# Performance work log

Measured on AMD Instinct MI355X. Metric: run time of the kernel, lower is better.

Reference implementation:

```python
import jax, jax.numpy as jnp
import numpy as np


def setup_inputs() -> dict:
    key = jax.random.key(0)
    k1, k2, k3, k4 = jax.random.split(key, 4)
    B, IN, OUT, R = 4096, 4096, 4096, 256
    x = jax.random.normal(k1, (B, IN), dtype=jnp.float32)
    U = jax.random.normal(k2, (R, IN), dtype=jnp.float32) / np.sqrt(IN)
    V = jax.random.normal(k3, (OUT, R), dtype=jnp.float32) / np.sqrt(R)
    bias = jax.random.uniform(k4, (OUT,), dtype=jnp.float32,
                              minval=-IN ** -0.5, maxval=IN ** -0.5)
    return {"x": x, "U": U, "V": V, "bias": bias}


def reference(x, U, V, bias):
    # Low-rank linear: out[b,j] = sum_k V[j,k] * (sum_i U[k,i] * x[b,i]) + bias[j]
    # (the torch loops with sparsity=1.0 / keep_stride==1 compute exactly this)
    t = jnp.einsum('bi,ri->br', x, U)        # [B, R]
    out = jnp.einsum('br,or->bo', t, V) + bias  # [B, OUT]
    return out
```

## Files before the change

### kernel.cpp

```cpp
#include <hip/hip_runtime.h>

typedef __attribute__((ext_vector_type(8))) short bf16x8;
typedef __attribute__((ext_vector_type(4))) float f32x4;

__device__ __forceinline__ unsigned short f2bf(float f) {
  unsigned int u = __float_as_uint(f);
  return (unsigned short)((u + 0x7fffu + ((u >> 16) & 1u)) >> 16);
}

__device__ __forceinline__ void gload_lds16(const void* g, void* l) {
  __builtin_amdgcn_global_load_lds((const __attribute__((address_space(1))) void*)g,
                                   (__attribute__((address_space(3))) void*)l,
                                   16, 0, 0);
}

__global__ void cast3(const float4* __restrict__ x, const float4* __restrict__ U,
                      const float4* __restrict__ V, ushort4* __restrict__ xb,
                      ushort4* __restrict__ Ub, ushort4* __restrict__ Vb) {
  const int NX = 4096 * 4096 / 4;
  const int NU = 256 * 4096 / 4;
  int i = blockIdx.x * blockDim.x + threadIdx.x;
  int stride = gridDim.x * blockDim.x;
  for (; i < NX + 2 * NU; i += stride) {
    const float4* s; ushort4* d; int j;
    if (i < NX)           { s = x; d = xb; j = i; }
    else if (i < NX + NU) { s = U; d = Ub; j = i - NX; }
    else                  { s = V; d = Vb; j = i - NX - NU; }
    float4 v = s[j];
    ushort4 o;
    o.x = f2bf(v.x); o.y = f2bf(v.y); o.z = f2bf(v.z); o.w = f2bf(v.w);
    d[j] = o;
  }
}

template <int MREP, int NREP, bool BIAS>
__global__ __launch_bounds__(256)
void gemm_nt(const unsigned short* __restrict__ A,
             const unsigned short* __restrict__ B,
             const float* __restrict__ bias,
             float* __restrict__ C,
             int lda, int ldb, int ldc,
             int nkt, int kChunk, long long splitStride) {
  constexpr int BM = 32 * MREP;
  constexpr int BN = 32 * NREP;
  constexpr int ISS_A = BM / 64;
  constexpr int ISS_B = BN / 64;

  __shared__ unsigned short sA[2][BM * 32];
  __shared__ unsigned short sB[2][BN * 32];

  const int tid = threadIdx.x;
  const int l = tid & 63;
  const int w = tid >> 6;
  const int wm = (w >> 1) * (MREP * 16);
  const int wn = (w & 1) * (NREP * 16);
  const int rm = blockIdx.x * BM;
  const int rn = blockIdx.y * BN;
  const int k0base = blockIdx.z * kChunk;

  const int lr = l & 15;
  const int lc8 = (l >> 4) * 8;

  auto stage = [&](int kt, int buf) {
    const int k0 = k0base + kt * 32;
#pragma unroll
    for (int is = 0; is < ISS_A; ++is) {
      int eo = is * 2048 + tid * 8;
      int r = eo >> 5, c = eo & 31;
      gload_lds16(A + (long long)(rm + r) * lda + k0 + c, &sA[buf][eo]);
    }
#pragma unroll
    for (int is = 0; is < ISS_B; ++is) {
      int eo = is * 2048 + tid * 8;
      int r = eo >> 5, c = eo & 31;
      gload_lds16(B + (long long)(rn + r) * ldb + k0 + c, &sB[buf][eo]);
    }
  };

  f32x4 acc[MREP][NREP] = {};

  stage(0, 0);
  for (int kt = 0; kt < nkt; ++kt) {
    __syncthreads();
    if (kt + 1 < nkt) stage(kt + 1, (kt + 1) & 1);
    const unsigned short* a0 = sA[kt & 1];
    const unsigned short* b0 = sB[kt & 1];
    bf16x8 af[MREP], bfr[NREP];
#pragma unroll
    for (int m = 0; m < MREP; ++m)
      af[m] = *(const bf16x8*)&a0[(wm + m * 16 + lr) * 32 + lc8];
#pragma unroll
    for (int n = 0; n < NREP; ++n)
      bfr[n] = *(const bf16x8*)&b0[(wn + n * 16 + lr) * 32 + lc8];
#pragma unroll
    for (int m = 0; m < MREP; ++m)
#pragma unroll
      for (int n = 0; n < NREP; ++n)
        acc[m][n] = __builtin_amdgcn_mfma_f32_16x16x32_bf16(af[m], bfr[n], acc[m][n], 0, 0, 0);
  }

  float* Cb = C + (long long)blockIdx.z * splitStride;
  const int r0 = rm + wm + (l >> 4) * 4;
  const int c0 = rn + wn + lr;
#pragma unroll
  for (int n = 0; n < NREP; ++n) {
    const int cc = c0 + n * 16;
    const float badd = BIAS ? bias[cc] : 0.0f;
#pragma unroll
    for (int m = 0; m < MREP; ++m) {
#pragma unroll
      for (int i = 0; i < 4; ++i)
        Cb[(long long)(r0 + m * 16 + i) * ldc + cc] = acc[m][n][i] + badd;
    }
  }
}

__global__ void reduce4(const float4* __restrict__ P, ushort4* __restrict__ t) {
  const int S = 4096 * 256 / 4;
  int i = blockIdx.x * 256 + threadIdx.x;
  float4 a = P[i], b = P[i + S], c = P[i + 2 * S], d = P[i + 3 * S];
  ushort4 o;
  o.x = f2bf(a.x + b.x + c.x + d.x);
  o.y = f2bf(a.y + b.y + c.y + d.y);
  o.z = f2bf(a.z + b.z + c.z + d.z);
  o.w = f2bf(a.w + b.w + c.w + d.w);
  t[i] = o;
}

extern "C" void kernel_launch(void* const* d_in, const int* in_sizes, int n_in,
                              void* d_out, int out_size, void* d_ws, size_t ws_size,
                              hipStream_t stream) {
  const float* x    = (const float*)d_in[0];
  const float* U    = (const float*)d_in[1];
  const float* V    = (const float*)d_in[2];
  const float* bias = (const float*)d_in[3];
  float* out = (float*)d_out;

  char* ws = (char*)d_ws;
  float* P            = (float*)ws;
  unsigned short* tb  = (unsigned short*)(ws + (16u << 20));
  unsigned short* xb  = (unsigned short*)(ws + (18u << 20));
  unsigned short* Ub  = (unsigned short*)(ws + (50u << 20));
  unsigned short* Vb  = (unsigned short*)(ws + (52u << 20));

  cast3<<<2048, 256, 0, stream>>>((const float4*)x, (const float4*)U, (const float4*)V,
                                  (ushort4*)xb, (ushort4*)Ub, (ushort4*)Vb);

  dim3 g1(4096 / 64, 256 / 128, 4);
  gemm_nt<2, 4, false><<<g1, 256, 0, stream>>>(xb, Ub, nullptr, P,
                                               4096, 4096, 256,
                                               32, 1024,
                                               (long long)4096 * 256);

  reduce4<<<(4096 * 256 / 4) / 256, 256, 0, stream>>>((const float4*)P, (ushort4*)tb);

  dim3 g2(4096 / 128, 4096 / 128, 1);
  gemm_nt<4, 4, true><<<g2, 256, 0, stream>>>(tb, Vb, bias, out,
                                              256, 256, 4096,
                                              8, 0, 0);
}
```

Measured before the change: 69.01 us.

## Fuse fp32-to-bf16 cast of x into first GEMM loads, widen split-K to 8

The separate cast pass over the large x matrix is removed. The first GEMM now reads fp32 x directly, converts it to bf16 in registers and stores it to LDS, which avoids writing and re-reading a bf16 copy of x. The first GEMM's tiling changes to 32x256 tiles with 8-way split-K, and the reduction kernel now sums 8 partials. The trade-off is that the A-side loads become synchronous register loads instead of direct global-to-LDS loads, and the partial-sum buffer doubles in size.

```diff
diff --git a/kernel.cpp b/kernel.cpp
--- a/kernel.cpp
+++ b/kernel.cpp
@@ -14,28 +14,22 @@
                                    16, 0, 0);
 }
 
-__global__ void cast3(const float4* __restrict__ x, const float4* __restrict__ U,
-                      const float4* __restrict__ V, ushort4* __restrict__ xb,
-                      ushort4* __restrict__ Ub, ushort4* __restrict__ Vb) {
-  const int NX = 4096 * 4096 / 4;
+__global__ void castUV(const float4* __restrict__ U, const float4* __restrict__ V,
+                       ushort4* __restrict__ Ub, ushort4* __restrict__ Vb) {
   const int NU = 256 * 4096 / 4;
-  int i = blockIdx.x * blockDim.x + threadIdx.x;
-  int stride = gridDim.x * blockDim.x;
-  for (; i < NX + 2 * NU; i += stride) {
-    const float4* s; ushort4* d; int j;
-    if (i < NX)           { s = x; d = xb; j = i; }
-    else if (i < NX + NU) { s = U; d = Ub; j = i - NX; }
-    else                  { s = V; d = Vb; j = i - NX - NU; }
-    float4 v = s[j];
-    ushort4 o;
-    o.x = f2bf(v.x); o.y = f2bf(v.y); o.z = f2bf(v.z); o.w = f2bf(v.w);
-    d[j] = o;
-  }
+  int i = blockIdx.x * 256 + threadIdx.x;
+  const float4* s; ushort4* d; int j;
+  if (i < NU) { s = U; d = Ub; j = i; }
+  else        { s = V; d = Vb; j = i - NU; }
+  float4 v = s[j];
+  ushort4 o;
+  o.x = f2bf(v.x); o.y = f2bf(v.y); o.z = f2bf(v.z); o.w = f2bf(v.w);
+  d[j] = o;
 }
 
-template <int MREP, int NREP, bool BIAS>
+template <int MREP, int NREP, bool BIAS, bool AFP32>
 __global__ __launch_bounds__(256)
-void gemm_nt(const unsigned short* __restrict__ A,
+void gemm_nt(const void* __restrict__ Ap,
              const unsigned short* __restrict__ B,
              const float* __restrict__ bias,
              float* __restrict__ C,
@@ -63,11 +57,34 @@
 
   auto stage = [&](int kt, int buf) {
     const int k0 = k0base + kt * 32;
+    if constexpr (AFP32) {
+      const float* A32 = (const float*)Ap;
+      constexpr int EPT = BM * 32 / 256;
+      const int eo = tid * EPT;
+      const int r = eo >> 5, c = eo & 31;
+      const float* src = A32 + (long long)(rm + r) * lda + k0 + c;
+      if constexpr (EPT == 4) {
+        float4 v = *(const float4*)src;
+        ushort4 o;
+        o.x = f2bf(v.x); o.y = f2bf(v.y); o.z = f2bf(v.z); o.w = f2bf(v.w);
+        *(ushort4*)&sA[buf][eo] = o;
+      } else {
+        float4 v0 = *(const float4*)src;
+        float4 v1 = *(const float4*)(src + 4);
+        ushort4 o0, o1;
+        o0.x = f2bf(v0.x); o0.y = f2bf(v0.y); o0.z = f2bf(v0.z); o0.w = f2bf(v0.w);
+        o1.x = f2bf(v1.x); o1.y = f2bf(v1.y); o1.z = f2bf(v1.z); o1.w = f2bf(v1.w);
+        *(ushort4*)&sA[buf][eo] = o0;
+        *(ushort4*)&sA[buf][eo + 4] = o1;
+      }
+    } else {
+      const unsigned short* A = (const unsigned short*)Ap;
 #pragma unroll
-    for (int is = 0; is < ISS_A; ++is) {
-      int eo = is * 2048 + tid * 8;
-      int r = eo >> 5, c = eo & 31;
-      gload_lds16(A + (long long)(rm + r) * lda + k0 + c, &sA[buf][eo]);
+      for (int is = 0; is < ISS_A; ++is) {
+        int eo = is * 2048 + tid * 8;
+        int r = eo >> 5, c = eo & 31;
+        gload_lds16(A + (long long)(rm + r) * lda + k0 + c, &sA[buf][eo]);
+      }
     }
 #pragma unroll
     for (int is = 0; is < ISS_B; ++is) {
@@ -115,15 +132,17 @@
   }
 }
 
-__global__ void reduce4(const float4* __restrict__ P, ushort4* __restrict__ t) {
+__global__ void reduce8(const float4* __restrict__ P, ushort4* __restrict__ t) {
   const int S = 4096 * 256 / 4;
   int i = blockIdx.x * 256 + threadIdx.x;
-  float4 a = P[i], b = P[i + S], c = P[i + 2 * S], d = P[i + 3 * S];
+  float4 s = P[i];
+#pragma unroll
+  for (int z = 1; z < 8; ++z) {
+    float4 v = P[i + z * S];
+    s.x += v.x; s.y += v.y; s.z += v.z; s.w += v.w;
+  }
   ushort4 o;
-  o.x = f2bf(a.x + b.x + c.x + d.x);
-  o.y = f2bf(a.y + b.y + c.y + d.y);
-  o.z = f2bf(a.z + b.z + c.z + d.z);
-  o.w = f2bf(a.w + b.w + c.w + d.w);
+  o.x = f2bf(s.x); o.y = f2bf(s.y); o.z = f2bf(s.z); o.w = f2bf(s.w);
   t[i] = o;
 }
 
@@ -138,24 +157,23 @@
 
   char* ws = (char*)d_ws;
   float* P            = (float*)ws;
-  unsigned short* tb  = (unsigned short*)(ws + (16u << 20));
-  unsigned short* xb  = (unsigned short*)(ws + (18u << 20));
-  unsigned short* Ub  = (unsigned short*)(ws + (50u << 20));
-  unsigned short* Vb  = (unsigned short*)(ws + (52u << 20));
+  unsigned short* tb  = (unsigned short*)(ws + (32u << 20));
+  unsigned short* Ub  = (unsigned short*)(ws + (34u << 20));
+  unsigned short* Vb  = (unsigned short*)(ws + (36u << 20));
 
-  cast3<<<2048, 256, 0, stream>>>((const float4*)x, (const float4*)U, (const float4*)V,
-                                  (ushort4*)xb, (ushort4*)Ub, (ushort4*)Vb);
+  castUV<<<2048, 256, 0, stream>>>((const float4*)U, (const float4*)V,
+                                   (ushort4*)Ub, (ushort4*)Vb);
 
-  dim3 g1(4096 / 64, 256 / 128, 4);
-  gemm_nt<2, 4, false><<<g1, 256, 0, stream>>>(xb, Ub, nullptr, P,
-                                               4096, 4096, 256,
-                                               32, 1024,
-                                               (long long)4096 * 256);
+  dim3 g1(4096 / 32, 1, 8);
+  gemm_nt<1, 8, false, true><<<g1, 256, 0, stream>>>(x, Ub, nullptr, P,
+                                                     4096, 4096, 256,
+                                                     16, 512,
+                                                     (long long)4096 * 256);
 
-  reduce4<<<(4096 * 256 / 4) / 256, 256, 0, stream>>>((const float4*)P, (ushort4*)tb);
+  reduce8<<<(4096 * 256 / 4) / 256, 256, 0, stream>>>((const float4*)P, (ushort4*)tb);
 
   dim3 g2(4096 / 128, 4096 / 128, 1);
-  gemm_nt<4, 4, true><<<g2, 256, 0, stream>>>(tb, Vb, bias, out,
-                                              256, 256, 4096,
-                                              8, 0, 0);
+  gemm_nt<4, 4, true, false><<<g2, 256, 0, stream>>>(tb, Vb, bias, out,
+                                                     256, 256, 4096,
+                                                     8, 0, 0);
 }
```

Result: no change. 67.94 us (-1.6%).
